# Performance work log

Measured on AMD Instinct MI355X. Metric: run time of the kernel, lower is better.

Reference implementation:

```python
import jax, jax.numpy as jnp
import numpy as np

N_NODES = 50000
N_EDGES = 1000000


def _gat_layer(x, edge_index, edge_prob, W, Wt, a_src, a_trg, a_tp, b, Wskip, concat):
    """One GATLayerImp3 forward (eval mode, dropout=identity).
    x: [N,Fin], edge_index: [2,E] (row0=src,row1=trg), edge_prob: [E,1].
    a_*: [1,H,F]. Returns [N,H*F] if concat else [N,F]."""
    N = x.shape[0]
    H, F = a_src.shape[1], a_src.shape[2]
    src, trg = edge_index[0], edge_index[1]

    proj = (x @ W).reshape(N, H, F)                      # [N,H,F]
    tp_proj = (edge_prob @ Wt).reshape(-1, H, F)         # [E,H,F]

    s_src = jnp.sum(proj * a_src, axis=-1)               # [N,H]
    s_trg = jnp.sum(proj * a_trg, axis=-1)               # [N,H]
    s_tp = jnp.sum(tp_proj * a_tp, axis=-1)              # [E,H]

    scores = jax.nn.leaky_relu(s_src[src] + s_trg[trg] + s_tp, 0.2)  # [E,H]
    exp_s = jnp.exp(scores - jnp.max(scores))            # global max, as in original
    denom = jax.ops.segment_sum(exp_s, trg, num_segments=N)[trg]     # [E,H]
    att = (exp_s / (denom + 1e-16))[:, :, None]          # [E,H,1]

    out = jax.ops.segment_sum(proj[src] * att, trg, num_segments=N)  # [N,H,F]

    if Wskip is None:  # dims match -> identity skip
        out = out + x[:, None, :]
    else:
        out = out + (x @ Wskip).reshape(N, H, F)

    out = out.reshape(N, H * F) if concat else out.mean(axis=1)
    return jax.nn.elu(out + b)


def setup_inputs() -> dict:
    key = jax.random.key(0)
    ks = jax.random.split(key, 16)
    s = 0.05
    return {
        "x": jax.random.normal(ks[0], (N_NODES, 128), jnp.float32),
        "edge_index": jax.random.randint(ks[1], (2, N_EDGES), 0, N_NODES, jnp.int32),
        "edge_prob": jax.random.uniform(ks[2], (N_EDGES, 1), jnp.float32),
        "W1": jax.random.normal(ks[3], (128, 128), jnp.float32) * s,
        "Wt1": jax.random.normal(ks[4], (1, 128), jnp.float32) * s,
        "a_src1": jax.random.normal(ks[5], (1, 8, 16), jnp.float32) * s,
        "a_trg1": jax.random.normal(ks[6], (1, 8, 16), jnp.float32) * s,
        "a_tp1": jax.random.normal(ks[7], (1, 8, 16), jnp.float32) * s,
        "b1": jnp.zeros((128,), jnp.float32),
        "Wskip1": jax.random.normal(ks[8], (128, 128), jnp.float32) * s,
        "W2": jax.random.normal(ks[9], (128, 128), jnp.float32) * s,
        "Wt2": jax.random.normal(ks[10], (1, 128), jnp.float32) * s,
        "a_src2": jax.random.normal(ks[11], (1, 1, 128), jnp.float32) * s,
        "a_trg2": jax.random.normal(ks[12], (1, 1, 128), jnp.float32) * s,
        "a_tp2": jax.random.normal(ks[13], (1, 1, 128), jnp.float32) * s,
        "b2": jnp.zeros((128,), jnp.float32),
    }


def reference(x, edge_index, edge_prob, W1, Wt1, a_src1, a_trg1, a_tp1, b1, Wskip1,
              W2, Wt2, a_src2, a_trg2, a_tp2, b2):
    h = _gat_layer(x, edge_index, edge_prob, W1, Wt1, a_src1, a_trg1, a_tp1, b1,
                   Wskip1, concat=True)                    # [N, 128]
    out = _gat_layer(h, edge_index, edge_prob, W2, Wt2, a_src2, a_trg2, a_tp2, b2,
                     None, concat=False)                   # [N, 128]
    return out
```

## Files before the change

kernel.cpp:

```cpp
#include <hip/hip_runtime.h>
#include <hip/hip_fp16.h>
#include <cstdint>
#include <cstddef>

typedef _Float16 half8 __attribute__((ext_vector_type(8)));
typedef float f32x4 __attribute__((ext_vector_type(4)));

__global__ void pack_b(const float* __restrict__ B, __half* __restrict__ Bp) {
  int slot = blockIdx.x * 256 + threadIdx.x;
  int lane = slot & 63;
  int nt = (slot >> 6) & 7;
  int kt = slot >> 9;
  int r0 = kt * 32 + (lane >> 4) * 8;
  int col = nt * 16 + (lane & 15);
  __half tmp[8];
#pragma unroll
  for (int j = 0; j < 8; ++j) tmp[j] = __float2half(B[(r0 + j) * 128 + col]);
  *reinterpret_cast<float4*>(Bp + (size_t)slot * 8) = *reinterpret_cast<float4*>(tmp);
}

__global__ void f32_to_f16(const float* __restrict__ in, __half* __restrict__ out, int n8) {
  int i = blockIdx.x * 256 + threadIdx.x;
  if (i >= n8) return;
  float4 a = *reinterpret_cast<const float4*>(in + (size_t)i * 8);
  float4 b = *reinterpret_cast<const float4*>(in + (size_t)i * 8 + 4);
  __half2 h[4] = {__floats2half2_rn(a.x, a.y), __floats2half2_rn(a.z, a.w),
                  __floats2half2_rn(b.x, b.y), __floats2half2_rn(b.z, b.w)};
  *reinterpret_cast<float4*>(out + (size_t)i * 8) = *reinterpret_cast<float4*>(h);
}

__global__ __launch_bounds__(256) void gemm_mfma(const __half* __restrict__ Ah,
                                                 const half8* __restrict__ Bp,
                                                 __half* __restrict__ C, int M) {
  const int w = threadIdx.x >> 6, lane = threadIdx.x & 63;
  const int row0 = blockIdx.x * 64 + w * 16;
  const int arow = row0 + (lane & 15);
  const int kb = (lane >> 4) * 8;
  const bool av = arow < M;
  f32x4 acc[8] = {};
  for (int kt = 0; kt < 4; ++kt) {
    half8 af = {};
    if (av) af = *reinterpret_cast<const half8*>(Ah + (size_t)arow * 128 + kt * 32 + kb);
    const half8* bb = Bp + (kt * 8) * 64 + lane;
#pragma unroll
    for (int nt = 0; nt < 8; ++nt)
      acc[nt] = __builtin_amdgcn_mfma_f32_16x16x32_f16(af, bb[nt * 64], acc[nt], 0, 0, 0);
  }
  const int orow = row0 + (lane >> 4) * 4;
  const int col = lane & 15;
#pragma unroll
  for (int r = 0; r < 4; ++r) {
    int rr = orow + r;
    if (rr < M) {
#pragma unroll
      for (int nt = 0; nt < 8; ++nt)
        C[(size_t)rr * 128 + nt * 16 + col] = __float2half(acc[nt][r]);
    }
  }
}

__global__ __launch_bounds__(256) void gemm_mfma_dual(const __half* __restrict__ Ah,
                                                      const half8* __restrict__ Bp1,
                                                      const half8* __restrict__ Bp2,
                                                      __half* __restrict__ C1,
                                                      __half* __restrict__ C2, int M) {
  const int w = threadIdx.x >> 6, lane = threadIdx.x & 63;
  const int row0 = blockIdx.x * 64 + w * 16;
  const int arow = row0 + (lane & 15);
  const int kb = (lane >> 4) * 8;
  const bool av = arow < M;
  f32x4 acc1[8] = {};
  f32x4 acc2[8] = {};
  for (int kt = 0; kt < 4; ++kt) {
    half8 af = {};
    if (av) af = *reinterpret_cast<const half8*>(Ah + (size_t)arow * 128 + kt * 32 + kb);
    const half8* b1 = Bp1 + (kt * 8) * 64 + lane;
    const half8* b2 = Bp2 + (kt * 8) * 64 + lane;
#pragma unroll
    for (int nt = 0; nt < 8; ++nt) {
      acc1[nt] = __builtin_amdgcn_mfma_f32_16x16x32_f16(af, b1[nt * 64], acc1[nt], 0, 0, 0);
      acc2[nt] = __builtin_amdgcn_mfma_f32_16x16x32_f16(af, b2[nt * 64], acc2[nt], 0, 0, 0);
    }
  }
  const int orow = row0 + (lane >> 4) * 4;
  const int col = lane & 15;
#pragma unroll
  for (int r = 0; r < 4; ++r) {
    int rr = orow + r;
    if (rr < M) {
#pragma unroll
      for (int nt = 0; nt < 8; ++nt) {
        C1[(size_t)rr * 128 + nt * 16 + col] = __float2half(acc1[nt][r]);
        C2[(size_t)rr * 128 + nt * 16 + col] = __float2half(acc2[nt][r]);
      }
    }
  }
}

__global__ __launch_bounds__(256) void bucket_hist(const int* __restrict__ trg,
                                                   int* __restrict__ bhist, int E) {
  __shared__ int cnt[256];
  cnt[threadIdx.x] = 0;
  __syncthreads();
  const int base = blockIdx.x * 1024;
#pragma unroll
  for (int j = 0; j < 4; ++j) {
    int e = base + threadIdx.x + j * 256;
    if (e < E) atomicAdd(&cnt[trg[e] >> 8], 1);
  }
  __syncthreads();
  int c = cnt[threadIdx.x];
  if (c) atomicAdd(&bhist[threadIdx.x], c);
}

__global__ void scan196(const int* __restrict__ bhist, int* __restrict__ boffx,
                        int* __restrict__ bcur, int* __restrict__ row_off, int nb, int N) {
  __shared__ int s[256];
  int t = threadIdx.x;
  bcur[t] = 0;
  int v = (t < nb) ? bhist[t] : 0;
  s[t] = v;
  __syncthreads();
#pragma unroll
  for (int off = 1; off < 256; off <<= 1) {
    int x = s[t];
    int add = (t >= off) ? s[t - off] : 0;
    __syncthreads();
    s[t] = x + add;
    __syncthreads();
  }
  if (t < nb) boffx[t] = (t == 0) ? 0 : s[t - 1];
  if (t == 0) {
    boffx[nb] = s[255];
    row_off[N] = s[255];
  }
}

__global__ __launch_bounds__(256) void bucket_scatter(
    const int* __restrict__ src, const int* __restrict__ trg,
    const float* __restrict__ ep, const int* __restrict__ boffx,
    int* __restrict__ bcur, int2* __restrict__ staging, int E, int N) {
  __shared__ int cnt[256], boff[256], rowb[256];
  const int nb2 = (N + 255) >> 8;
  if (threadIdx.x < nb2) cnt[threadIdx.x] = 0;
  __syncthreads();
  const int base = blockIdx.x * 1024;
  int b_[4], r_[4], s_[4], p_[4];
#pragma unroll
  for (int j = 0; j < 4; ++j) {
    int e = base + threadIdx.x + j * 256;
    bool v = e < E;
    int tg = v ? trg[e] : 0;
    int sc = v ? src[e] : 0;
    p_[j] = v ? __float_as_int(ep[e]) : 0;
    b_[j] = tg >> 8;
    s_[j] = sc | ((tg & 255) << 16);
    r_[j] = v ? atomicAdd(&cnt[b_[j]], 1) : -1;
  }
  __syncthreads();
  if (threadIdx.x < nb2) {
    int c = cnt[threadIdx.x];
    boff[threadIdx.x] = c ? atomicAdd(&bcur[threadIdx.x], c) : 0;
    rowb[threadIdx.x] = boffx[threadIdx.x];
  }
  __syncthreads();
#pragma unroll
  for (int j = 0; j < 4; ++j) {
    if (r_[j] >= 0) {
      int b = b_[j];
      staging[rowb[b] + boff[b] + r_[j]] = make_int2(s_[j], p_[j]);
    }
  }
}

__global__ __launch_bounds__(256) void bucket_place(
    const int2* __restrict__ staging, const int* __restrict__ boffx,
    int* __restrict__ row_off, int2* __restrict__ edge2, int N) {
  __shared__ int cnt[256], loc[256], cur[256];
  const int t = threadIdx.x;
  const int n0 = blockIdx.x << 8;
  const int nn = min(256, N - n0);
  cnt[t] = 0;
  __syncthreads();
  const int lo = boffx[blockIdx.x];
  const int hi = boffx[blockIdx.x + 1];
  for (int i = lo + t; i < hi; i += 256) {
    atomicAdd(&cnt[(staging[i].x >> 16) & 255], 1);
  }
  __syncthreads();
  loc[t] = cnt[t];
  __syncthreads();
#pragma unroll
  for (int off = 1; off < 256; off <<= 1) {
    int x = loc[t];
    int add = (t >= off) ? loc[t - off] : 0;
    __syncthreads();
    loc[t] = x + add;
    __syncthreads();
  }
  int excl = loc[t] - cnt[t];
  if (t < nn) row_off[n0 + t] = lo + excl;
  cur[t] = lo + excl;
  __syncthreads();
  for (int i = lo + t; i < hi; i += 256) {
    int2 v = staging[i];
    int ln = (v.x >> 16) & 255;
    int pos = atomicAdd(&cur[ln], 1);
    edge2[pos] = make_int2(v.x & 0xFFFF, v.y);
  }
}

template <int H, int F>
__global__ void node_scores_h(const __half* __restrict__ projh, const float* __restrict__ a_src,
                              const float* __restrict__ a_trg, float* __restrict__ ssrc,
                              float* __restrict__ strg, int N) {
  int idx = blockIdx.x * blockDim.x + threadIdx.x;
  if (idx >= N * H) return;
  int n = idx / H, h = idx % H;
  const __half* p = projh + (size_t)n * (H * F) + h * F;
  const float* as = a_src + h * F;
  const float* at = a_trg + h * F;
  float d1 = 0.f, d2 = 0.f;
#pragma unroll
  for (int f = 0; f < F; f += 8) {
    float4 raw = *reinterpret_cast<const float4*>(p + f);
    const __half2* hp = reinterpret_cast<const __half2*>(&raw);
    float2 p01 = __half22float2(hp[0]);
    float2 p23 = __half22float2(hp[1]);
    float2 p45 = __half22float2(hp[2]);
    float2 p67 = __half22float2(hp[3]);
    float4 a0 = *reinterpret_cast<const float4*>(as + f);
    float4 a1 = *reinterpret_cast<const float4*>(as + f + 4);
    float4 t0 = *reinterpret_cast<const float4*>(at + f);
    float4 t1 = *reinterpret_cast<const float4*>(at + f + 4);
    d1 += p01.x * a0.x + p01.y * a0.y + p23.x * a0.z + p23.y * a0.w +
          p45.x * a1.x + p45.y * a1.y + p67.x * a1.z + p67.y * a1.w;
    d2 += p01.x * t0.x + p01.y * t0.y + p23.x * t0.z + p23.y * t0.w +
          p45.x * t1.x + p45.y * t1.y + p67.x * t1.z + p67.y * t1.w;
  }
  ssrc[idx] = d1;
  strg[idx] = d2;
}

template <int H, int F, bool OUT_F16>
__global__ void aggregate(const int2* __restrict__ edge2, const int* __restrict__ row_off,
                          const float* __restrict__ ssrc, const float* __restrict__ strg,
                          const float* __restrict__ Wt, const float* __restrict__ a_tp,
                          const __half* __restrict__ projh, const __half* __restrict__ skiph,
                          const float* __restrict__ bias, void* __restrict__ outv, int N) {
  static_assert(H * F == 128, "offset shift assumes H*F==128");
  int wid = (blockIdx.x * blockDim.x + threadIdx.x) >> 6;
  if (wid >= N) return;
  const int lane = threadIdx.x & 63;
  const int half = lane >> 5;
  const int fl = (lane & 31) * 4;
  const int h = fl / F;

  float4 wt4 = *reinterpret_cast<const float4*>(Wt + fl);
  float4 at4 = *reinterpret_cast<const float4*>(a_tp + fl);
  float ch = wt4.x * at4.x + wt4.y * at4.y + wt4.z * at4.z + wt4.w * at4.w;
#pragma unroll
  for (int off = 1; off < (F / 4); off <<= 1) ch += __shfl_xor(ch, off);

  const float mt = strg[wid * H + h];
  const int beg = row_off[wid];
  const int end = row_off[wid + 1];

  float ax = 0.f, ay = 0.f, az = 0.f, aw = 0.f;
  float denom = 0.f;

  for (int i = beg; i < end; i += 8) {
    int   s[4];
    float pe[4], vd[4];
    float2 raw[4];
#pragma unroll
    for (int q = 0; q < 4; ++q) {
      int ii = i + q * 2 + half;
      bool v = ii < end;
      int2 e2 = v ? edge2[ii] : make_int2(0, 0);
      s[q] = e2.x;
      pe[q] = __int_as_float(e2.y);
      vd[q] = v ? 1.f : 0.f;
    }
#pragma unroll
    for (int q = 0; q < 4; ++q)
      raw[q] = *reinterpret_cast<const float2*>(projh + (s[q] << 7) + fl);
#pragma unroll
    for (int q = 0; q < 4; ++q) {
      float sc = ssrc[s[q] * H + h] + mt + pe[q] * ch;
      sc = sc > 0.f ? sc : 0.2f * sc;
      float ee = __expf(sc) * vd[q];
      __half2 h01 = *reinterpret_cast<__half2*>(&raw[q].x);
      __half2 h23 = *reinterpret_cast<__half2*>(&raw[q].y);
      float2 f01 = __half22float2(h01);
      float2 f23 = __half22float2(h23);
      denom += ee;
      ax += f01.x * ee;
      ay += f01.y * ee;
      az += f23.x * ee;
      aw += f23.y * ee;
    }
  }

  denom += __shfl_xor(denom, 32);
  ax += __shfl_xor(ax, 32);
  ay += __shfl_xor(ay, 32);
  az += __shfl_xor(az, 32);
  aw += __shfl_xor(aw, 32);

  if (half == 0) {
    float inv = 1.0f / (denom + 1e-16f);
    int base = (wid << 7) + fl;
    float2 skraw = *reinterpret_cast<const float2*>(skiph + base);
    const __half2* sp = reinterpret_cast<const __half2*>(&skraw);
    float2 s01 = __half22float2(sp[0]);
    float2 s23 = __half22float2(sp[1]);
    float4 bi = *reinterpret_cast<const float4*>(bias + fl);
    float o0 = ax * inv + s01.x + bi.x;
    float o1 = ay * inv + s01.y + bi.y;
    float o2 = az * inv + s23.x + bi.z;
    float o3 = aw * inv + s23.y + bi.w;
    o0 = o0 > 0.f ? o0 : __expf(o0) - 1.f;
    o1 = o1 > 0.f ? o1 : __expf(o1) - 1.f;
    o2 = o2 > 0.f ? o2 : __expf(o2) - 1.f;
    o3 = o3 > 0.f ? o3 : __expf(o3) - 1.f;
    if (OUT_F16) {
      __half2 w01 = __floats2half2_rn(o0, o1);
      __half2 w23 = __floats2half2_rn(o2, o3);
      float2 wv;
      reinterpret_cast<__half2*>(&wv)[0] = w01;
      reinterpret_cast<__half2*>(&wv)[1] = w23;
      *reinterpret_cast<float2*>(reinterpret_cast<__half*>(outv) + base) = wv;
    } else {
      *reinterpret_cast<float4*>(reinterpret_cast<float*>(outv) + base) =
          make_float4(o0, o1, o2, o3);
    }
  }
}

extern "C" void kernel_launch(void* const* d_in, const int* in_sizes, int n_in,
                              void* d_out, int out_size, void* d_ws, size_t ws_size,
                              hipStream_t stream) {
  const float* x      = (const float*)d_in[0];
  const int*   ei     = (const int*)  d_in[1];
  const float* ep     = (const float*)d_in[2];
  const float* W1     = (const float*)d_in[3];
  const float* Wt1    = (const float*)d_in[4];
  const float* a_src1 = (const float*)d_in[5];
  const float* a_trg1 = (const float*)d_in[6];
  const float* a_tp1  = (const float*)d_in[7];
  const float* b1     = (const float*)d_in[8];
  const float* Wskip1 = (const float*)d_in[9];
  const float* W2     = (const float*)d_in[10];
  const float* Wt2    = (const float*)d_in[11];
  const float* a_src2 = (const float*)d_in[12];
  const float* a_trg2 = (const float*)d_in[13];
  const float* a_tp2  = (const float*)d_in[14];
  const float* b2     = (const float*)d_in[15];

  const int N = in_sizes[0] / 128;
  const int E = in_sizes[1] / 2;
  const int* srcA = ei;
  const int* trgA = ei + E;

  char* ws = (char*)d_ws;
  size_t off = 0;
  auto alloc = [&](size_t bytes) {
    void* p = ws + off;
    off += (bytes + 255) & ~(size_t)255;
    return p;
  };
  int*    bhist   = (int*)   alloc((size_t)256 * 4);
  int*    bcur    = (int*)   alloc((size_t)256 * 4);
  int*    boffx   = (int*)   alloc((size_t)257 * 4);
  int*    row_off = (int*)   alloc((size_t)(N + 1) * 4);
  int2*   staging = (int2*)  alloc((size_t)E * 8);
  int2*   edge2   = (int2*)  alloc((size_t)E * 8);
  __half* xh      = (__half*)alloc((size_t)N * 128 * 2);
  __half* projh   = (__half*)alloc((size_t)N * 128 * 2);
  __half* skiph   = (__half*)alloc((size_t)N * 128 * 2);
  __half* hbufh   = (__half*)alloc((size_t)N * 128 * 2);
  __half* Bp1     = (__half*)alloc((size_t)2048 * 8 * 2);
  __half* BpS     = (__half*)alloc((size_t)2048 * 8 * 2);
  __half* Bp2     = (__half*)alloc((size_t)2048 * 8 * 2);
  float*  ssrc    = (float*) alloc((size_t)N * 8 * 4);
  float*  strg    = (float*) alloc((size_t)N * 8 * 4);
  (void)ws_size; (void)n_in; (void)out_size;

  hipMemsetAsync(bhist, 0, 256 * 4, stream);

  const int eb4 = (E + 1023) / 1024;
  const int gb = (N + 63) / 64;
  const int nb = (N + 255) / 256;

  f32_to_f16<<<(N * 16 + 255) / 256, 256, 0, stream>>>(x, xh, N * 16);
  pack_b<<<8, 256, 0, stream>>>(W1, Bp1);
  pack_b<<<8, 256, 0, stream>>>(Wskip1, BpS);
  pack_b<<<8, 256, 0, stream>>>(W2, Bp2);

  bucket_hist<<<eb4, 256, 0, stream>>>(trgA, bhist, E);
  scan196<<<1, 256, 0, stream>>>(bhist, boffx, bcur, row_off, nb, N);
  bucket_scatter<<<eb4, 256, 0, stream>>>(srcA, trgA, ep, boffx, bcur, staging, E, N);
  bucket_place<<<nb, 256, 0, stream>>>(staging, boffx, row_off, edge2, N);

  gemm_mfma_dual<<<gb, 256, 0, stream>>>(xh, (const half8*)Bp1, (const half8*)BpS,
                                         projh, skiph, N);
  node_scores_h<8, 16><<<(N * 8 + 255) / 256, 256, 0, stream>>>(projh, a_src1, a_trg1,
                                                                ssrc, strg, N);
  aggregate<8, 16, true><<<(N + 3) / 4, 256, 0, stream>>>(edge2, row_off, ssrc, strg, Wt1,
                                                          a_tp1, projh, skiph, b1, hbufh, N);

  gemm_mfma<<<gb, 256, 0, stream>>>(hbufh, (const half8*)Bp2, projh, N);
  node_scores_h<1, 128><<<(N + 255) / 256, 256, 0, stream>>>(projh, a_src2, a_trg2,
                                                             ssrc, strg, N);
  aggregate<1, 128, false><<<(N + 3) / 4, 256, 0, stream>>>(edge2, row_off, ssrc, strg, Wt2,
                                                            a_tp2, projh, hbufh, b2,
                                                            (float*)d_out, N);
}
```

Measured before the change: 344.8 us.

## Fuse attention score dot products into GEMM epilogues and merge weight packing

Computes the per-node source and target attention scores inside the GEMM epilogues from the fp32 accumulators, using 16-lane shuffle reductions. This removes the two node_scores kernels and their re-read of the fp16 projections. The three weight-packing launches become one, and the aggregation loop is unrolled to 8 edge pairs per iteration so more gathers are in flight. The costs are extra shuffles and registers in the GEMM epilogue, higher register pressure in aggregate, and scores now computed from fp32 rather than fp16-rounded projections.

```diff
diff --git a/kernel.cpp b/kernel.cpp
--- a/kernel.cpp
+++ b/kernel.cpp
@@ -6,8 +6,13 @@
 typedef _Float16 half8 __attribute__((ext_vector_type(8)));
 typedef float f32x4 __attribute__((ext_vector_type(4)));
 
-__global__ void pack_b(const float* __restrict__ B, __half* __restrict__ Bp) {
-  int slot = blockIdx.x * 256 + threadIdx.x;
+__global__ void pack_b3(const float* __restrict__ B1, const float* __restrict__ BS,
+                        const float* __restrict__ B2, __half* __restrict__ Bp1,
+                        __half* __restrict__ BpS, __half* __restrict__ Bp2) {
+  int g = blockIdx.x >> 3;
+  const float* B = (g == 0) ? B1 : (g == 1) ? BS : B2;
+  __half* Bp = (g == 0) ? Bp1 : (g == 1) ? BpS : Bp2;
+  int slot = (blockIdx.x & 7) * 256 + threadIdx.x;
   int lane = slot & 63;
   int nt = (slot >> 6) & 7;
   int kt = slot >> 9;
@@ -29,41 +34,11 @@
   *reinterpret_cast<float4*>(out + (size_t)i * 8) = *reinterpret_cast<float4*>(h);
 }
 
-__global__ __launch_bounds__(256) void gemm_mfma(const __half* __restrict__ Ah,
-                                                 const half8* __restrict__ Bp,
-                                                 __half* __restrict__ C, int M) {
-  const int w = threadIdx.x >> 6, lane = threadIdx.x & 63;
-  const int row0 = blockIdx.x * 64 + w * 16;
-  const int arow = row0 + (lane & 15);
-  const int kb = (lane >> 4) * 8;
-  const bool av = arow < M;
-  f32x4 acc[8] = {};
-  for (int kt = 0; kt < 4; ++kt) {
-    half8 af = {};
-    if (av) af = *reinterpret_cast<const half8*>(Ah + (size_t)arow * 128 + kt * 32 + kb);
-    const half8* bb = Bp + (kt * 8) * 64 + lane;
-#pragma unroll
-    for (int nt = 0; nt < 8; ++nt)
-      acc[nt] = __builtin_amdgcn_mfma_f32_16x16x32_f16(af, bb[nt * 64], acc[nt], 0, 0, 0);
-  }
-  const int orow = row0 + (lane >> 4) * 4;
-  const int col = lane & 15;
-#pragma unroll
-  for (int r = 0; r < 4; ++r) {
-    int rr = orow + r;
-    if (rr < M) {
-#pragma unroll
-      for (int nt = 0; nt < 8; ++nt)
-        C[(size_t)rr * 128 + nt * 16 + col] = __float2half(acc[nt][r]);
-    }
-  }
-}
-
-__global__ __launch_bounds__(256) void gemm_mfma_dual(const __half* __restrict__ Ah,
-                                                      const half8* __restrict__ Bp1,
-                                                      const half8* __restrict__ Bp2,
-                                                      __half* __restrict__ C1,
-                                                      __half* __restrict__ C2, int M) {
+__global__ __launch_bounds__(256) void gemm_mfma_dual(
+    const __half* __restrict__ Ah, const half8* __restrict__ Bp1,
+    const half8* __restrict__ Bp2, const float* __restrict__ a_src,
+    const float* __restrict__ a_trg, __half* __restrict__ C1, __half* __restrict__ C2,
+    float* __restrict__ ssrc, float* __restrict__ strg, int M) {
   const int w = threadIdx.x >> 6, lane = threadIdx.x & 63;
   const int row0 = blockIdx.x * 64 + w * 16;
   const int arow = row0 + (lane & 15);
@@ -84,15 +59,89 @@
   }
   const int orow = row0 + (lane >> 4) * 4;
   const int col = lane & 15;
+  float asv[8], atv[8];
+#pragma unroll
+  for (int h2 = 0; h2 < 8; ++h2) {
+    asv[h2] = a_src[h2 * 16 + col];
+    atv[h2] = a_trg[h2 * 16 + col];
+  }
 #pragma unroll
   for (int r = 0; r < 4; ++r) {
     int rr = orow + r;
-    if (rr < M) {
-#pragma unroll
-      for (int nt = 0; nt < 8; ++nt) {
-        C1[(size_t)rr * 128 + nt * 16 + col] = __float2half(acc1[nt][r]);
-        C2[(size_t)rr * 128 + nt * 16 + col] = __float2half(acc2[nt][r]);
+    if (rr >= M) continue;
+#pragma unroll
+    for (int nt = 0; nt < 8; ++nt) {
+      C1[(size_t)rr * 128 + nt * 16 + col] = __float2half(acc1[nt][r]);
+      C2[(size_t)rr * 128 + nt * 16 + col] = __float2half(acc2[nt][r]);
+    }
+    float sv[8], tv[8];
+#pragma unroll
+    for (int h2 = 0; h2 < 8; ++h2) {
+      sv[h2] = acc1[h2][r] * asv[h2];
+      tv[h2] = acc1[h2][r] * atv[h2];
+    }
+#pragma unroll
+    for (int off = 1; off < 16; off <<= 1) {
+#pragma unroll
+      for (int h2 = 0; h2 < 8; ++h2) {
+        sv[h2] += __shfl_xor(sv[h2], off);
+        tv[h2] += __shfl_xor(tv[h2], off);
       }
+    }
+    if (col == 0) {
+      *reinterpret_cast<float4*>(ssrc + rr * 8) = make_float4(sv[0], sv[1], sv[2], sv[3]);
+      *reinterpret_cast<float4*>(ssrc + rr * 8 + 4) = make_float4(sv[4], sv[5], sv[6], sv[7]);
+      *reinterpret_cast<float4*>(strg + rr * 8) = make_float4(tv[0], tv[1], tv[2], tv[3]);
+      *reinterpret_cast<float4*>(strg + rr * 8 + 4) = make_float4(tv[4], tv[5], tv[6], tv[7]);
+    }
+  }
+}
+
+__global__ __launch_bounds__(256) void gemm_mfma_s(
+    const __half* __restrict__ Ah, const half8* __restrict__ Bp,
+    const float* __restrict__ a_src, const float* __restrict__ a_trg,
+    __half* __restrict__ C, float* __restrict__ ssrc, float* __restrict__ strg, int M) {
+  const int w = threadIdx.x >> 6, lane = threadIdx.x & 63;
+  const int row0 = blockIdx.x * 64 + w * 16;
+  const int arow = row0 + (lane & 15);
+  const int kb = (lane >> 4) * 8;
+  const bool av = arow < M;
+  f32x4 acc[8] = {};
+  for (int kt = 0; kt < 4; ++kt) {
+    half8 af = {};
+    if (av) af = *reinterpret_cast<const half8*>(Ah + (size_t)arow * 128 + kt * 32 + kb);
+    const half8* bb = Bp + (kt * 8) * 64 + lane;
+#pragma unroll
+    for (int nt = 0; nt < 8; ++nt)
+      acc[nt] = __builtin_amdgcn_mfma_f32_16x16x32_f16(af, bb[nt * 64], acc[nt], 0, 0, 0);
+  }
+  const int orow = row0 + (lane >> 4) * 4;
+  const int col = lane & 15;
+  float asv[8], atv[8];
+#pragma unroll
+  for (int nt = 0; nt < 8; ++nt) {
+    asv[nt] = a_src[nt * 16 + col];
+    atv[nt] = a_trg[nt * 16 + col];
+  }
+#pragma unroll
+  for (int r = 0; r < 4; ++r) {
+    int rr = orow + r;
+    if (rr >= M) continue;
+    float sp = 0.f, tp = 0.f;
+#pragma unroll
+    for (int nt = 0; nt < 8; ++nt) {
+      C[(size_t)rr * 128 + nt * 16 + col] = __float2half(acc[nt][r]);
+      sp += acc[nt][r] * asv[nt];
+      tp += acc[nt][r] * atv[nt];
+    }
+#pragma unroll
+    for (int off = 1; off < 16; off <<= 1) {
+      sp += __shfl_xor(sp, off);
+      tp += __shfl_xor(tp, off);
+    }
+    if (col == 0) {
+      ssrc[rr] = sp;
+      strg[rr] = tp;
     }
   }
 }
@@ -208,38 +257,6 @@
     int pos = atomicAdd(&cur[ln], 1);
     edge2[pos] = make_int2(v.x & 0xFFFF, v.y);
   }
-}
-
-template <int H, int F>
-__global__ void node_scores_h(const __half* __restrict__ projh, const float* __restrict__ a_src,
-                              const float* __restrict__ a_trg, float* __restrict__ ssrc,
-                              float* __restrict__ strg, int N) {
-  int idx = blockIdx.x * blockDim.x + threadIdx.x;
-  if (idx >= N * H) return;
-  int n = idx / H, h = idx % H;
-  const __half* p = projh + (size_t)n * (H * F) + h * F;
-  const float* as = a_src + h * F;
-  const float* at = a_trg + h * F;
-  float d1 = 0.f, d2 = 0.f;
-#pragma unroll
-  for (int f = 0; f < F; f += 8) {
-    float4 raw = *reinterpret_cast<const float4*>(p + f);
-    const __half2* hp = reinterpret_cast<const __half2*>(&raw);
-    float2 p01 = __half22float2(hp[0]);
-    float2 p23 = __half22float2(hp[1]);
-    float2 p45 = __half22float2(hp[2]);
-    float2 p67 = __half22float2(hp[3]);
-    float4 a0 = *reinterpret_cast<const float4*>(as + f);
-    float4 a1 = *reinterpret_cast<const float4*>(as + f + 4);
-    float4 t0 = *reinterpret_cast<const float4*>(at + f);
-    float4 t1 = *reinterpret_cast<const float4*>(at + f + 4);
-    d1 += p01.x * a0.x + p01.y * a0.y + p23.x * a0.z + p23.y * a0.w +
-          p45.x * a1.x + p45.y * a1.y + p67.x * a1.z + p67.y * a1.w;
-    d2 += p01.x * t0.x + p01.y * t0.y + p23.x * t0.z + p23.y * t0.w +
-          p45.x * t1.x + p45.y * t1.y + p67.x * t1.z + p67.y * t1.w;
-  }
-  ssrc[idx] = d1;
-  strg[idx] = d2;
 }
 
 template <int H, int F, bool OUT_F16>
@@ -269,12 +286,12 @@
   float ax = 0.f, ay = 0.f, az = 0.f, aw = 0.f;
   float denom = 0.f;
 
-  for (int i = beg; i < end; i += 8) {
-    int   s[4];
-    float pe[4], vd[4];
-    float2 raw[4];
-#pragma unroll
-    for (int q = 0; q < 4; ++q) {
+  for (int i = beg; i < end; i += 16) {
+    int   s[8];
+    float pe[8], vd[8];
+    float2 raw[8];
+#pragma unroll
+    for (int q = 0; q < 8; ++q) {
       int ii = i + q * 2 + half;
       bool v = ii < end;
       int2 e2 = v ? edge2[ii] : make_int2(0, 0);
@@ -283,10 +300,10 @@
       vd[q] = v ? 1.f : 0.f;
     }
 #pragma unroll
-    for (int q = 0; q < 4; ++q)
+    for (int q = 0; q < 8; ++q)
       raw[q] = *reinterpret_cast<const float2*>(projh + (s[q] << 7) + fl);
 #pragma unroll
-    for (int q = 0; q < 4; ++q) {
+    for (int q = 0; q < 8; ++q) {
       float sc = ssrc[s[q] * H + h] + mt + pe[q] * ch;
       sc = sc > 0.f ? sc : 0.2f * sc;
       float ee = __expf(sc) * vd[q];
@@ -394,9 +411,7 @@
   const int nb = (N + 255) / 256;
 
   f32_to_f16<<<(N * 16 + 255) / 256, 256, 0, stream>>>(x, xh, N * 16);
-  pack_b<<<8, 256, 0, stream>>>(W1, Bp1);
-  pack_b<<<8, 256, 0, stream>>>(Wskip1, BpS);
-  pack_b<<<8, 256, 0, stream>>>(W2, Bp2);
+  pack_b3<<<24, 256, 0, stream>>>(W1, Wskip1, W2, Bp1, BpS, Bp2);
 
   bucket_hist<<<eb4, 256, 0, stream>>>(trgA, bhist, E);
   scan196<<<1, 256, 0, stream>>>(bhist, boffx, bcur, row_off, nb, N);
@@ -404,15 +419,12 @@
   bucket_place<<<nb, 256, 0, stream>>>(staging, boffx, row_off, edge2, N);
 
   gemm_mfma_dual<<<gb, 256, 0, stream>>>(xh, (const half8*)Bp1, (const half8*)BpS,
-                                         projh, skiph, N);
-  node_scores_h<8, 16><<<(N * 8 + 255) / 256, 256, 0, stream>>>(projh, a_src1, a_trg1,
-                                                                ssrc, strg, N);
+                                         a_src1, a_trg1, projh, skiph, ssrc, strg, N);
   aggregate<8, 16, true><<<(N + 3) / 4, 256, 0, stream>>>(edge2, row_off, ssrc, strg, Wt1,
                                                           a_tp1, projh, skiph, b1, hbufh, N);
 
-  gemm_mfma<<<gb, 256, 0, stream>>>(hbufh, (const half8*)Bp2, projh, N);
-  node_scores_h<1, 128><<<(N + 255) / 256, 256, 0, stream>>>(projh, a_src2, a_trg2,
-                                                             ssrc, strg, N);
+  gemm_mfma_s<<<gb, 256, 0, stream>>>(hbufh, (const half8*)Bp2, a_src2, a_trg2,
+                                      projh, ssrc, strg, N);
   aggregate<1, 128, false><<<(N + 3) / 4, 256, 0, stream>>>(edge2, row_off, ssrc, strg, Wt2,
                                                             a_tp2, projh, hbufh, b2,
                                                             (float*)d_out, N);
```

New measurement: 342.1 us. No clear change (-0.8%).
